# Kernel tuning notes

Measured on AMD Instinct MI355X. Metric: run time of the kernel, lower is better.

## Reference

```python
import math
import jax, jax.numpy as jnp
import numpy as np

B, T, N, FIN, D, H, HM, L, P, O = 8, 12, 512, 3, 128, 4, 256, 3, 12, 1


def _pe(t, d):
    pos = jnp.arange(t, dtype=jnp.float32)[:, None]
    div = jnp.exp(jnp.arange(0, d, 2, dtype=jnp.float32) * (-math.log(10000.0) / d))
    pe = jnp.zeros((t, d), jnp.float32)
    pe = pe.at[:, 0::2].set(jnp.sin(pos * div))
    pe = pe.at[:, 1::2].set(jnp.cos(pos * div))
    return pe


def _spatial_attn(x, qkvW, qkvb, pW, pb):
    # attention over the node axis, per (batch, time)
    b, t, n, d = x.shape
    hd = d // H
    scale = hd ** -0.5
    qkv = jnp.einsum('btnd,ced->cbtne', x, qkvW) + qkvb[:, None, None, None, :]
    q, k, v = [a.reshape(b, t, n, H, hd) for a in qkv]
    a = jax.nn.softmax(jnp.einsum('btihe,btjhe->bthij', q, k) * scale, axis=-1)
    o = jnp.einsum('bthij,btjhe->btihe', a, v).reshape(b, t, n, d)
    return jnp.einsum('btnd,od->btno', o, pW) + pb


def _temporal_attn(x, qkvW, qkvb, pW, pb):
    # attention over the time axis, per (batch, node)
    b, t, n, d = x.shape
    hd = d // H
    scale = hd ** -0.5
    qkv = jnp.einsum('btnd,ced->cbtne', x, qkvW) + qkvb[:, None, None, None, :]
    q, k, v = [a.reshape(b, t, n, H, hd) for a in qkv]
    a = jax.nn.softmax(jnp.einsum('bxnhe,bynhe->bnhxy', q, k) * scale, axis=-1)
    o = jnp.einsum('bnhxy,bynhe->bxnhe', a, v).reshape(b, t, n, d)
    return jnp.einsum('btnd,od->btno', o, pW) + pb


def _layernorm(x, g, b, eps=1e-5):
    mu = x.mean(-1, keepdims=True)
    var = ((x - mu) ** 2).mean(-1, keepdims=True)
    return (x - mu) / jnp.sqrt(var + eps) * g + b


def setup_inputs() -> dict:
    key = jax.random.key(0)
    ks = iter(jax.random.split(key, 40))
    s = 0.02
    rn = lambda shape: jax.random.normal(next(ks), shape, jnp.float32) * s
    inp = {
        'x': jax.random.normal(next(ks), (B, T, N, FIN), jnp.float32),
        'tok_W': rn((D, FIN)), 'tok_b': rn((D,)),
        't_qkvW': rn((L, 3, D, D)), 't_qkvb': rn((L, 3, D)),
        't_pW': rn((L, D, D)), 't_pb': rn((L, D)),
        'g_qkvW': rn((L, 3, D, D)), 'g_qkvb': rn((L, 3, D)),
        'g_pW': rn((L, D, D)), 'g_pb': rn((L, D)),
        's_qkvW': rn((L, 3, D, D)), 's_qkvb': rn((L, 3, D)),
        's_pW': rn((L, D, D)), 's_pb': rn((L, D)),
        'resW': rn((L, D, D)), 'resb': rn((L, D)),
        'normW': jnp.ones((L, D), jnp.float32), 'normb': jnp.zeros((L, D), jnp.float32),
        'fc1W': rn((L, HM, 2 * D)), 'fc1b': rn((L, HM)),
        'fc2W': rn((L, D, HM)), 'fc2b': rn((L, D)),
        'end1W': rn((P, T)), 'end1b': rn((P,)),
        'end2W': rn((O, L * D)), 'end2b': rn((O,)),
    }
    return inp


def reference(x, tok_W, tok_b, t_qkvW, t_qkvb, t_pW, t_pb,
              g_qkvW, g_qkvb, g_pW, g_pb, s_qkvW, s_qkvb, s_pW, s_pb,
              resW, resb, normW, normb, fc1W, fc1b, fc2W, fc2b,
              end1W, end1b, end2W, end2b):
    # DataEmbedding: token linear + sinusoidal positional encoding over T
    h = jnp.einsum('btnf,df->btnd', x, tok_W) + tok_b
    h = h + _pe(h.shape[1], h.shape[3])[None, :, None, :]
    outs = []
    for l in range(t_qkvW.shape[0]):
        residual = h
        h = _temporal_attn(h, t_qkvW[l], t_qkvb[l], t_pW[l], t_pb[l])
        geo = _spatial_attn(h, g_qkvW[l], g_qkvb[l], g_pW[l], g_pb[l])
        sem = _spatial_attn(h, s_qkvW[l], s_qkvb[l], s_pW[l], s_pb[l])
        cat = jnp.concatenate([geo, sem], axis=-1)
        m = jax.nn.gelu(jnp.einsum('btnc,hc->btnh', cat, fc1W[l]) + fc1b[l], approximate=False)
        m = jnp.einsum('btnh,oh->btno', m, fc2W[l]) + fc2b[l]
        pre = jnp.einsum('btnd,od->btno', residual, resW[l]) + resb[l] + m
        h = _layernorm(pre, normW[l], normb[l])
        outs.append(h)
    xc = jnp.concatenate(outs, axis=-1)  # [B,T,N,L*D]
    y = jax.nn.relu(jnp.einsum('btnc,pt->bpnc', xc, end1W) + end1b[None, :, None, None])
    y = jnp.einsum('bpnc,oc->bpno', y, end2W) + end2b
    return y  # [B, pred_len, N, output_size]; structure_kl_loss is identically 0
```

## Files before the change

kernel.cpp:

```cpp
#include <hip/hip_runtime.h>
#include <hip/hip_bf16.h>
#include <math.h>

#define BB 8
#define TT 12
#define NN 512
#define FIN 3
#define DD 128
#define HH 4
#define HD 32
#define HMID 256
#define LL 3
#define PP 12
#define BTOK (TT*NN)

typedef short bf16x8 __attribute__((ext_vector_type(8)));
typedef float f32x4  __attribute__((ext_vector_type(4)));

__device__ __forceinline__ unsigned short f2bf(float f) {
    unsigned u = __float_as_uint(f);
    unsigned r = u + 0x7fffu + ((u >> 16) & 1u);
    return (unsigned short)(r >> 16);
}
__device__ __forceinline__ float bf2f(short s) {
    return __uint_as_float((unsigned)(unsigned short)s << 16);
}
__device__ __forceinline__ unsigned pk2bf(float a, float b) {
    __hip_bfloat162 h = __float22bfloat162_rn(make_float2(a, b));
    return *(unsigned*)&h;
}

__global__ __launch_bounds__(256)
void convert_weights_kernel(const float* __restrict__ t_qkvW, const float* __restrict__ t_pW,
                            const float* __restrict__ g_qkvW, const float* __restrict__ g_pW,
                            const float* __restrict__ s_qkvW, const float* __restrict__ s_pW,
                            const float* __restrict__ resW, const float* __restrict__ fc1W,
                            const float* __restrict__ fc2W, short* __restrict__ dst)
{
    int base = (blockIdx.x * 256 + threadIdx.x) * 4;
    const float* src; int off;
    if      (base < 147456) { src = t_qkvW; off = 0; }
    else if (base < 196608) { src = t_pW;   off = 147456; }
    else if (base < 344064) { src = g_qkvW; off = 196608; }
    else if (base < 393216) { src = g_pW;   off = 344064; }
    else if (base < 540672) { src = s_qkvW; off = 393216; }
    else if (base < 589824) { src = s_pW;   off = 540672; }
    else if (base < 638976) { src = resW;   off = 589824; }
    else if (base < 835584) { src = fc1W;   off = 638976; }
    else                    { src = fc2W;   off = 835584; }
    float4 v = *(const float4*)(src + (base - off));
    *(uint2*)(dst + base) = make_uint2(pk2bf(v.x, v.y), pk2bf(v.z, v.w));
}

__global__ __launch_bounds__(256)
void combine_weights_kernel(const float* __restrict__ g_qkvW, const float* __restrict__ s_qkvW,
                            const float* __restrict__ t_pW, const float* __restrict__ g_pW,
                            const float* __restrict__ s_pW, const float* __restrict__ g_qkvb,
                            const float* __restrict__ s_qkvb, const float* __restrict__ t_pb,
                            const float* __restrict__ g_pb, const float* __restrict__ s_pb,
                            const float* __restrict__ fc1W, const float* __restrict__ fc1b,
                            short* __restrict__ wbf, float* __restrict__ qkvb2,
                            float* __restrict__ fc1b2)
{
    __shared__ float Bs[128][128];
    const int tid = threadIdx.x;
    const int blk = blockIdx.x;
    const float* A; const float* B; int arst;
    short* outp; int orst;
    int l, sel, c = 0, half = 0;
    const bool isqkv = blk < 18;
    if (isqkv) {
        l = blk / 6; int r = blk % 6; sel = r / 3; c = r % 3;
        A = (sel ? s_qkvW : g_qkvW) + (size_t)(l*3 + c) * 16384;  arst = 128;
        B = t_pW + (size_t)l * 16384;
        outp = wbf + (sel ? 393216 : 196608) + (size_t)l*49152 + (size_t)c*16384;
        orst = 128;
    } else {
        int r = blk - 18; l = r / 4; r %= 4; sel = r >> 1; half = r & 1;
        A = fc1W + (size_t)(l*256 + half*128) * 256 + sel*128;    arst = 256;
        B = (sel ? s_pW : g_pW) + (size_t)l * 16384;
        outp = wbf + 638976 + (size_t)l*65536 + (size_t)half*32768 + sel*128;
        orst = 256;
    }
    for (int idx = tid; idx < 16384; idx += 256)
        Bs[idx >> 7][idx & 127] = B[idx];
    __syncthreads();

    const int e = tid >> 1, db = (tid & 1) * 64;
    const float* Arow = A + (size_t)e * arst;
    #pragma unroll 1
    for (int ch = 0; ch < 4; ++ch) {
        float acc[16] = {};
        for (int o4 = 0; o4 < 32; ++o4) {
            float4 a4 = *(const float4*)(Arow + o4*4);
            float as[4] = {a4.x, a4.y, a4.z, a4.w};
            #pragma unroll
            for (int k = 0; k < 4; ++k) {
                #pragma unroll
                for (int j4 = 0; j4 < 4; ++j4) {
                    float4 b = *(const float4*)&Bs[o4*4 + k][db + ch*16 + j4*4];
                    acc[j4*4+0] += as[k]*b.x;
                    acc[j4*4+1] += as[k]*b.y;
                    acc[j4*4+2] += as[k]*b.z;
                    acc[j4*4+3] += as[k]*b.w;
                }
            }
        }
        short* orow = outp + (size_t)e * orst + db + ch*16;
        #pragma unroll
        for (int j = 0; j < 8; ++j)
            ((unsigned*)orow)[j] = pk2bf(acc[2*j], acc[2*j+1]);
    }

    if (tid < 128) {
        if (isqkv) {
            const float* tb = t_pb + l*128;
            const float* ar = A + (size_t)tid * 128;
            float s = (sel ? s_qkvb : g_qkvb)[(l*3 + c)*128 + tid];
            for (int o = 0; o < 128; ++o) s += ar[o] * tb[o];
            qkvb2[l*768 + sel*384 + c*128 + tid] = s;
        } else if (sel == 0) {
            int hg = half*128 + tid;
            const float* frow = fc1W + (size_t)(l*256 + hg) * 256;
            const float* gb = g_pb + l*128;
            const float* sb = s_pb + l*128;
            float s = fc1b[l*256 + hg];
            for (int o = 0; o < 128; ++o) s += frow[o]*gb[o] + frow[128+o]*sb[o];
            fc1b2[l*256 + hg] = s;
        }
    }
}

__global__ __launch_bounds__(256)
void embed_kernel(const float* __restrict__ x, const float* __restrict__ tokW,
                  const float* __restrict__ tokb, short* __restrict__ h)
{
    int gid = blockIdx.x * 256 + threadIdx.x;
    int d = gid & (DD - 1);
    int token = gid >> 7;
    int t = (token / NN) % TT;
    const float* xp = x + (size_t)token * FIN;
    float v = tokb[d] + xp[0]*tokW[d*3+0] + xp[1]*tokW[d*3+1] + xp[2]*tokW[d*3+2];
    int de = d & ~1;
    float freq = __expf(-(float)de * (9.210340371976184f / (float)DD));
    float ang = (float)t * freq;
    v += (d & 1) ? cosf(ang) : sinf(ang);
    h[gid] = (short)f2bf(v);
}

template<int ACT, bool OBF16>
__device__ __forceinline__ void gemm_core(
    const short* __restrict__ Ap, int lda, const short* __restrict__ W, int K,
    const float* __restrict__ bias, const float* __restrict__ addsrc, int ald,
    void* __restrict__ outp, int ldc)
{
    __shared__ __align__(16) short As[64][72];
    __shared__ __align__(16) short Bs[128][72];
    const int tid = threadIdx.x;
    const int lane = tid & 63, w = tid >> 6;
    const int wm = (w & 1) * 32, wn = (w >> 1) * 64;
    const int l15 = lane & 15, lq = lane >> 4;
    f32x4 acc[2][4] = {};
    const int arow = tid >> 2, achk = (tid & 3) * 16;
    const int brow = tid >> 1, bchk = (tid & 1) * 32;

    for (int k0 = 0; k0 < K; k0 += 64) {
        const short* ap = Ap + (size_t)arow * lda + k0 + achk;
        *(uint4*)&As[arow][achk]     = *(const uint4*)ap;
        *(uint4*)&As[arow][achk + 8] = *(const uint4*)(ap + 8);
        const short* wp = W + (size_t)brow * K + k0 + bchk;
        #pragma unroll
        for (int i = 0; i < 4; ++i)
            *(uint4*)&Bs[brow][bchk + i*8] = *(const uint4*)(wp + i*8);
        __syncthreads();
        #pragma unroll
        for (int kc = 0; kc < 2; ++kc) {
            bf16x8 af[2], bfv[4];
            #pragma unroll
            for (int mi = 0; mi < 2; ++mi)
                af[mi] = *(const bf16x8*)&As[wm + mi*16 + l15][kc*32 + lq*8];
            #pragma unroll
            for (int nj = 0; nj < 4; ++nj)
                bfv[nj] = *(const bf16x8*)&Bs[wn + nj*16 + l15][kc*32 + lq*8];
            #pragma unroll
            for (int mi = 0; mi < 2; ++mi)
                #pragma unroll
                for (int nj = 0; nj < 4; ++nj)
                    acc[mi][nj] = __builtin_amdgcn_mfma_f32_16x16x32_bf16(
                        af[mi], bfv[nj], acc[mi][nj], 0, 0, 0);
        }
        __syncthreads();
    }

    #pragma unroll
    for (int nj = 0; nj < 4; ++nj) {
        int col = wn + nj * 16 + l15;
        float bv = bias[col];
        #pragma unroll
        for (int mi = 0; mi < 2; ++mi) {
            #pragma unroll
            for (int r = 0; r < 4; ++r) {
                int row = wm + mi * 16 + lq * 4 + r;
                float v = acc[mi][nj][r] + bv;
                if (addsrc) v += addsrc[(size_t)row * ald + col];
                if (ACT == 1) v = 0.5f * v * (1.0f + erff(v * 0.7071067811865476f));
                if (OBF16) ((short*)outp)[(size_t)row * ldc + col] = (short)f2bf(v);
                else       ((float*)outp)[(size_t)row * ldc + col] = v;
            }
        }
    }
}

template<int ACT, bool OBF16>
__global__ __launch_bounds__(256)
void gemm_plain(const short* __restrict__ A, const short* __restrict__ W,
                const float* __restrict__ bias, const float* __restrict__ addsrc,
                void* __restrict__ out, int K, int lda, int ldc, int ald)
{
    size_t bm = (size_t)blockIdx.x * 64;
    int bn = blockIdx.y * 128;
    void* op = OBF16 ? (void*)((short*)out + bm * ldc + bn)
                     : (void*)((float*)out + bm * ldc + bn);
    const float* ad = addsrc ? addsrc + bm * ald + bn : nullptr;
    gemm_core<ACT, OBF16>(A + bm * lda, lda, W + (size_t)bn * K, K, bias + bn,
                          ad, ald, op, ldc);
}

__global__ __launch_bounds__(256)
void gemm_qkv_gs(const short* __restrict__ A, const short* __restrict__ W1,
                 const short* __restrict__ W2, const float* __restrict__ b1,
                 const float* __restrict__ b2, short* __restrict__ out)
{
    size_t bm = (size_t)blockIdx.x * 64;
    int y = blockIdx.y;
    const short* W = (y < 3) ? W1 : W2;
    const float* b = (y < 3) ? b1 : b2;
    int wc = ((y < 3) ? y : y - 3) * 128;
    gemm_core<0, true>(A + bm * 128, 128, W + (size_t)wc * 128, 128,
                       b + wc, nullptr, 0, out + bm * 768 + y * 128, 768);
}

__global__ __launch_bounds__(192)
void temporal_attn_kernel(const short* __restrict__ qkv, short* __restrict__ out)
{
    __shared__ __align__(16) short kvs[4][TT][264];
    const int tid = threadIdx.x;
    const int bn0 = blockIdx.x * 4;

    #pragma unroll
    for (int i = 0; i < 8; ++i) {
        int flat = (i*192 + tid) * 8;
        int ns = flat / 3072;
        int rem = flat - ns*3072;
        int t = rem >> 8, c = rem & 255;
        int bn = bn0 + ns;
        int b = bn >> 9, n = bn & (NN - 1);
        const short* src = qkv + ((size_t)(b*TT + t) * NN + n) * 384 + 128 + c;
        *(uint4*)&kvs[ns][t][c] = *(const uint4*)src;
    }

    const int nsub = tid / 48;
    const int r = tid - nsub*48;
    const int h = r / TT, ti = r - h*TT;
    const int bn = bn0 + nsub;
    const int b = bn >> 9, n = bn & (NN - 1);
    const float qscale = 0.17677669529663687f * 1.4426950408889634f;

    float q[32];
    {
        const short* qp = qkv + ((size_t)(b*TT + ti) * NN + n) * 384 + h*HD;
        #pragma unroll
        for (int i = 0; i < 16; ++i) {
            unsigned u = ((const unsigned*)qp)[i];
            q[2*i]   = __uint_as_float(u << 16) * qscale;
            q[2*i+1] = __uint_as_float(u & 0xffff0000u) * qscale;
        }
    }
    __syncthreads();

    float s[TT];
    #pragma unroll
    for (int tj = 0; tj < TT; ++tj) {
        const unsigned* kr = (const unsigned*)&kvs[nsub][tj][h*HD];
        float d0 = 0.f, d1 = 0.f;
        #pragma unroll
        for (int i = 0; i < 16; ++i) {
            unsigned u = kr[i];
            d0 += q[2*i]   * __uint_as_float(u << 16);
            d1 += q[2*i+1] * __uint_as_float(u & 0xffff0000u);
        }
        s[tj] = d0 + d1;
    }
    float sum = 0.f, p[TT];
    #pragma unroll
    for (int tj = 0; tj < TT; ++tj) { p[tj] = __builtin_amdgcn_exp2f(s[tj]); sum += p[tj]; }
    float inv = 1.f / sum;

    float o[32];
    #pragma unroll
    for (int e = 0; e < 32; ++e) o[e] = 0.f;
    #pragma unroll
    for (int tj = 0; tj < TT; ++tj) {
        const unsigned* vr = (const unsigned*)&kvs[nsub][tj][128 + h*HD];
        float pj = p[tj];
        #pragma unroll
        for (int i = 0; i < 16; ++i) {
            unsigned u = vr[i];
            o[2*i]   += pj * __uint_as_float(u << 16);
            o[2*i+1] += pj * __uint_as_float(u & 0xffff0000u);
        }
    }

    short* op = out + ((size_t)(b*TT + ti) * NN + n) * DD + h*HD;
    #pragma unroll
    for (int i = 0; i < 16; ++i)
        ((unsigned*)op)[i] = pk2bf(o[2*i] * inv, o[2*i+1] * inv);
}

__global__ __launch_bounds__(256)
void spatial_attn_mfma_kernel(const short* __restrict__ qkv, short* __restrict__ out)
{
    __shared__ __align__(16) short Qs[128][40];
    __shared__ __align__(16) short Ks[64][40];
    __shared__ __align__(16) short Vt[36][72];
    __shared__ __align__(16) short Ps[4][32][72];

    const int tid = threadIdx.x;
    const int bid = blockIdx.x;
    const int sel = bid & 1;
    const int qb = (bid >> 1) & 3;
    const int h = (bid >> 3) & 3;
    const int bt = bid >> 5;
    const int lane = tid & 63, w = tid >> 6;
    const int l15 = lane & 15, lq = lane >> 4;

    const size_t btbase = (size_t)bt * NN * 768 + sel * 384 + h * HD;
    const float qscale = 0.17677669529663687f * 1.4426950408889634f;

    {
        int r = tid >> 1, hf = (tid & 1) * 16;
        const unsigned* qp = (const unsigned*)(qkv + btbase + (size_t)(qb*128 + r) * 768 + hf);
        unsigned tmp[8];
        #pragma unroll
        for (int i = 0; i < 8; ++i) {
            unsigned u = qp[i];
            tmp[i] = pk2bf(__uint_as_float(u << 16) * qscale,
                           __uint_as_float(u & 0xffff0000u) * qscale);
        }
        *(uint4*)&Qs[r][hf]     = *(const uint4*)tmp;
        *(uint4*)&Qs[r][hf + 8] = *(const uint4*)(tmp + 4);
    }
    for (int idx = tid; idx < 4*72; idx += 256) {
        int rr = idx / 72, cc = idx - rr*72;
        Vt[32 + rr][cc] = (rr == 0 && cc < 64) ? (short)0x3F80 : (short)0;
    }

    f32x4 acc_o[2][3] = {};
    const int ve = tid & 31, vkb = (tid >> 5) * 8;

    for (int kt = 0; kt < 8; ++kt) {
        __syncthreads();
        {
            int r = tid >> 2, c = (tid & 3) * 8;
            const short* kp = qkv + btbase + (size_t)(kt*64 + r) * 768 + 128 + c;
            *(uint4*)&Ks[r][c] = *(const uint4*)kp;
        }
        {
            const short* vp = qkv + btbase + (size_t)(kt*64 + vkb) * 768 + 256 + ve;
            short tmp[8];
            #pragma unroll
            for (int jj = 0; jj < 8; ++jj) tmp[jj] = vp[(size_t)jj * 768];
            *(uint4*)&Vt[ve][vkb] = *(const uint4*)tmp;
        }
        __syncthreads();

        bf16x8 kf[4], qf[2];
        #pragma unroll
        for (int km = 0; km < 4; ++km)
            kf[km] = *(const bf16x8*)&Ks[km*16 + l15][lq*8];
        #pragma unroll
        for (int qn = 0; qn < 2; ++qn)
            qf[qn] = *(const bf16x8*)&Qs[w*32 + qn*16 + l15][lq*8];
        f32x4 sacc[4][2] = {};
        #pragma unroll
        for (int km = 0; km < 4; ++km)
            #pragma unroll
            for (int qn = 0; qn < 2; ++qn)
                sacc[km][qn] = __builtin_amdgcn_mfma_f32_16x16x32_bf16(
                    kf[km], qf[qn], sacc[km][qn], 0, 0, 0);

        #pragma unroll
        for (int km = 0; km < 4; ++km)
            #pragma unroll
            for (int qn = 0; qn < 2; ++qn) {
                float e0 = __builtin_amdgcn_exp2f(sacc[km][qn][0]);
                float e1 = __builtin_amdgcn_exp2f(sacc[km][qn][1]);
                float e2 = __builtin_amdgcn_exp2f(sacc[km][qn][2]);
                float e3 = __builtin_amdgcn_exp2f(sacc[km][qn][3]);
                *(uint2*)&Ps[w][qn*16 + l15][km*16 + lq*4] =
                    make_uint2(pk2bf(e0, e1), pk2bf(e2, e3));
            }

        #pragma unroll
        for (int kk = 0; kk < 2; ++kk) {
            bf16x8 pa[2], vb[3];
            #pragma unroll
            for (int mi = 0; mi < 2; ++mi)
                pa[mi] = *(const bf16x8*)&Ps[w][mi*16 + l15][kk*32 + lq*8];
            #pragma unroll
            for (int nj = 0; nj < 3; ++nj)
                vb[nj] = *(const bf16x8*)&Vt[nj*16 + l15][kk*32 + lq*8];
            #pragma unroll
            for (int mi = 0; mi < 2; ++mi)
                #pragma unroll
                for (int nj = 0; nj < 3; ++nj)
                    acc_o[mi][nj] = __builtin_amdgcn_mfma_f32_16x16x32_bf16(
                        pa[mi], vb[nj], acc_o[mi][nj], 0, 0, 0);
        }
    }

    #pragma unroll
    for (int mi = 0; mi < 2; ++mi) {
        #pragma unroll
        for (int r = 0; r < 4; ++r) {
            float l = __shfl(acc_o[mi][2][r], lane & 48);
            float inv = 1.f / l;
            int qrow = qb*128 + w*32 + mi*16 + lq*4 + r;
            short* op = out + ((size_t)bt * NN + qrow) * 256 + sel*128 + h*HD;
            op[l15]      = (short)f2bf(acc_o[mi][0][r] * inv);
            op[16 + l15] = (short)f2bf(acc_o[mi][1][r] * inv);
        }
    }
}

__global__ __launch_bounds__(256)
void layernorm_kernel(const float* __restrict__ in, const float* __restrict__ g,
                      const float* __restrict__ bta, short* __restrict__ outh,
                      float* __restrict__ xc, int lcol)
{
    int tid = threadIdx.x;
    int wave = tid >> 6, lane = tid & 63;
    size_t token = (size_t)blockIdx.x * 4 + wave;
    const float* row = in + token * DD;
    float x0 = row[lane], x1 = row[lane + 64];
    float s = x0 + x1, ss = x0*x0 + x1*x1;
    #pragma unroll
    for (int off = 1; off < 64; off <<= 1) {
        s  += __shfl_xor(s,  off);
        ss += __shfl_xor(ss, off);
    }
    float mu = s * (1.f / DD);
    float var = ss * (1.f / DD) - mu * mu;
    float rstd = rsqrtf(var + 1e-5f);
    float y0 = (x0 - mu) * rstd * g[lane]      + bta[lane];
    float y1 = (x1 - mu) * rstd * g[lane + 64] + bta[lane + 64];
    outh[token*DD + lane]      = (short)f2bf(y0);
    outh[token*DD + lane + 64] = (short)f2bf(y1);
    xc[token*(LL*DD) + lcol + lane]      = y0;
    xc[token*(LL*DD) + lcol + lane + 64] = y1;
}

__global__ __launch_bounds__(256)
void head_kernel(const float* __restrict__ xc, const float* __restrict__ e1W,
                 const float* __restrict__ e1b, const float* __restrict__ e2W,
                 const float* __restrict__ e2b, float* __restrict__ out)
{
    __shared__ float xcs[TT][LL*DD];
    __shared__ float w1[PP*TT];
    int bid = blockIdx.x;
    int b = bid >> 9, n = bid & (NN - 1);
    int tid = threadIdx.x;
    if (tid < PP*TT) w1[tid] = e1W[tid];
    #pragma unroll
    for (int i = 0; i < 18; ++i) {
        int f = i*256 + tid;
        int t = f / (LL*DD), c = f % (LL*DD);
        xcs[t][c] = xc[(((size_t)(b*TT + t) * NN) + n) * (LL*DD) + c];
    }
    __syncthreads();
    int p = tid >> 4, lane16 = tid & 15;
    float acc = 0.f;
    if (p < PP) {
        for (int c = lane16; c < LL*DD; c += 16) {
            float tmp = e1b[p];
            #pragma unroll
            for (int t = 0; t < TT; ++t) tmp += xcs[t][c] * w1[p*TT + t];
            tmp = fmaxf(tmp, 0.f);
            acc += tmp * e2W[c];
        }
    }
    acc += __shfl_xor(acc, 1);
    acc += __shfl_xor(acc, 2);
    acc += __shfl_xor(acc, 4);
    acc += __shfl_xor(acc, 8);
    if (p < PP && lane16 == 0)
        out[((size_t)(b*PP + p)) * NN + n] = acc + e2b[0];
}

extern "C" void kernel_launch(void* const* d_in, const int* in_sizes, int n_in,
                              void* d_out, int out_size, void* d_ws, size_t ws_size,
                              hipStream_t stream)
{
    const float* x      = (const float*)d_in[0];
    const float* tok_W  = (const float*)d_in[1];
    const float* tok_b  = (const float*)d_in[2];
    const float* t_qkvW = (const float*)d_in[3];
    const float* t_qkvb = (const float*)d_in[4];
    const float* t_pW   = (const float*)d_in[5];
    const float* t_pb   = (const float*)d_in[6];
    const float* g_qkvW = (const float*)d_in[7];
    const float* g_qkvb = (const float*)d_in[8];
    const float* g_pW   = (const float*)d_in[9];
    const float* g_pb   = (const float*)d_in[10];
    const float* s_qkvW = (const float*)d_in[11];
    const float* s_qkvb = (const float*)d_in[12];
    const float* s_pW   = (const float*)d_in[13];
    const float* s_pb   = (const float*)d_in[14];
    const float* resW   = (const float*)d_in[15];
    const float* resb   = (const float*)d_in[16];
    const float* normW  = (const float*)d_in[17];
    const float* normb  = (const float*)d_in[18];
    const float* fc1W   = (const float*)d_in[19];
    const float* fc1b   = (const float*)d_in[20];
    const float* fc2W   = (const float*)d_in[21];
    const float* fc2b   = (const float*)d_in[22];
    const float* end1W  = (const float*)d_in[23];
    const float* end1b  = (const float*)d_in[24];
    const float* end2W  = (const float*)d_in[25];
    const float* end2b  = (const float*)d_in[26];
    float* out = (float*)d_out;

    short* wbf = (short*)d_ws;
    const size_t WBF = 933888;
    float* qkvb2 = (float*)(wbf + WBF);
    float* fc1b2 = qkvb2 + 2304;
    short* act   = (short*)(fc1b2 + 768);

    convert_weights_kernel<<<912, 256, 0, stream>>>(
        t_qkvW, t_pW, g_qkvW, g_pW, s_qkvW, s_pW, resW, fc1W, fc2W, wbf);
    combine_weights_kernel<<<30, 256, 0, stream>>>(
        g_qkvW, s_qkvW, t_pW, g_pW, s_pW, g_qkvb, s_qkvb, t_pb, g_pb, s_pb,
        fc1W, fc1b, wbf, qkvb2, fc1b2);

    const size_t fixedBytes = WBF*2 + 3072*4;
    const size_t perBatchBytes = (size_t)BTOK * 2432 * 2;
    int nb = 8;
    while (nb > 1 && fixedBytes + (size_t)nb * perBatchBytes > ws_size) nb >>= 1;

    for (int b0 = 0; b0 < BB; b0 += nb) {
        const int CT = nb * BTOK;
        const int GM = CT / 64;
        short* h    = act;
        short* qkvh = h + (size_t)CT*128;
        short* m1   = qkvh;
        short* atmp = qkvh + (size_t)CT*768;
        float* m2   = (float*)(atmp + (size_t)CT*256);
        float* pre  = m2 + (size_t)CT*128;
        float* xc   = pre + (size_t)CT*128;

        const float* xch = x + (size_t)b0 * BTOK * FIN;
        float* outch = out + (size_t)b0 * PP * NN;

        embed_kernel<<<CT*DD/256, 256, 0, stream>>>(xch, tok_W, tok_b, h);

        for (int l = 0; l < LL; ++l) {
            const short* tqw = wbf + 0      + (size_t)l*49152;
            const short* gqw = wbf + 196608 + (size_t)l*49152;
            const short* sqw = wbf + 393216 + (size_t)l*49152;
            const short* rsw = wbf + 589824 + (size_t)l*16384;
            const short* f1w = wbf + 638976 + (size_t)l*65536;
            const short* f2w = wbf + 835584 + (size_t)l*32768;
            const float* tqb = t_qkvb + (size_t)l*384;

            gemm_plain<0,true><<<dim3(GM,3), 256, 0, stream>>>(
                h, tqw, tqb, nullptr, qkvh, 128, 128, 384, 0);
            temporal_attn_kernel<<<nb*NN/4, 192, 0, stream>>>(qkvh, atmp);

            gemm_qkv_gs<<<dim3(GM,6), 256, 0, stream>>>(
                atmp, gqw, sqw, qkvb2 + l*768, qkvb2 + l*768 + 384, qkvh);
            spatial_attn_mfma_kernel<<<nb*TT*HH*4*2, 256, 0, stream>>>(qkvh, atmp);

            gemm_plain<1,true><<<dim3(GM,2), 256, 0, stream>>>(
                atmp, f1w, fc1b2 + l*256, nullptr, m1, 256, 256, 256, 0);
            gemm_plain<0,false><<<dim3(GM,1), 256, 0, stream>>>(
                m1, f2w, fc2b + (size_t)l*128, nullptr, m2, 256, 256, 128, 0);
            gemm_plain<0,false><<<dim3(GM,1), 256, 0, stream>>>(
                h, rsw, resb + (size_t)l*128, m2, pre, 128, 128, 128, 128);
            layernorm_kernel<<<CT/4, 256, 0, stream>>>(pre, normW + (size_t)l*128,
                                                       normb + (size_t)l*128, h, xc, l*DD);
        }

        head_kernel<<<nb*NN, 256, 0, stream>>>(xc, end1W, end1b, end2W, end2b, outch);
    }
}
```

Before: 769.5 us.

## Fuse fc2, residual projection and layernorm into one K-concatenated GEMM kernel

Lays out the fc1 output and the hidden state side by side in a single [token,384] buffer and builds a combined [fc2W | resW] weight. One GEMM with K=384 then computes fc2 plus the residual projection, and its epilogue applies LayerNorm directly. This removes two GEMM launches, the fp32 m2 and pre intermediates, and the separate layernorm pass. It also pads the spatial-attention shared-memory tiles, likely to reduce bank conflicts. The cost is a cross-wave reduction through shared memory inside the GEMM epilogue, and in-place overwriting of the hidden-state columns of the shared buffer.

```diff
diff --git a/kernel.cpp b/kernel.cpp
--- a/kernel.cpp
+++ b/kernel.cpp
@@ -38,6 +38,16 @@
                             const float* __restrict__ fc2W, short* __restrict__ dst)
 {
     int base = (blockIdx.x * 256 + threadIdx.x) * 4;
+    if (base >= 933888) {
+        int idx = base - 933888;
+        int l = idx / 49152, r2 = idx - l*49152;
+        int d = r2 / 384, col = r2 - d*384;
+        const float* s2 = (col < 256) ? fc2W + ((size_t)(l*128 + d))*256 + col
+                                      : resW + ((size_t)(l*128 + d))*128 + (col - 256);
+        float4 v = *(const float4*)s2;
+        *(uint2*)(dst + base) = make_uint2(pk2bf(v.x, v.y), pk2bf(v.z, v.w));
+        return;
+    }
     const float* src; int off;
     if      (base < 147456) { src = t_qkvW; off = 0; }
     else if (base < 196608) { src = t_pW;   off = 147456; }
@@ -133,7 +143,7 @@
 
 __global__ __launch_bounds__(256)
 void embed_kernel(const float* __restrict__ x, const float* __restrict__ tokW,
-                  const float* __restrict__ tokb, short* __restrict__ h)
+                  const float* __restrict__ tokb, short* __restrict__ cat2)
 {
     int gid = blockIdx.x * 256 + threadIdx.x;
     int d = gid & (DD - 1);
@@ -145,14 +155,13 @@
     float freq = __expf(-(float)de * (9.210340371976184f / (float)DD));
     float ang = (float)t * freq;
     v += (d & 1) ? cosf(ang) : sinf(ang);
-    h[gid] = (short)f2bf(v);
+    cat2[(size_t)token * 384 + 256 + d] = (short)f2bf(v);
 }
 
 template<int ACT, bool OBF16>
 __device__ __forceinline__ void gemm_core(
     const short* __restrict__ Ap, int lda, const short* __restrict__ W, int K,
-    const float* __restrict__ bias, const float* __restrict__ addsrc, int ald,
-    void* __restrict__ outp, int ldc)
+    const float* __restrict__ bias, void* __restrict__ outp, int ldc)
 {
     __shared__ __align__(16) short As[64][72];
     __shared__ __align__(16) short Bs[128][72];
@@ -202,7 +211,6 @@
             for (int r = 0; r < 4; ++r) {
                 int row = wm + mi * 16 + lq * 4 + r;
                 float v = acc[mi][nj][r] + bv;
-                if (addsrc) v += addsrc[(size_t)row * ald + col];
                 if (ACT == 1) v = 0.5f * v * (1.0f + erff(v * 0.7071067811865476f));
                 if (OBF16) ((short*)outp)[(size_t)row * ldc + col] = (short)f2bf(v);
                 else       ((float*)outp)[(size_t)row * ldc + col] = v;
@@ -214,16 +222,14 @@
 template<int ACT, bool OBF16>
 __global__ __launch_bounds__(256)
 void gemm_plain(const short* __restrict__ A, const short* __restrict__ W,
-                const float* __restrict__ bias, const float* __restrict__ addsrc,
-                void* __restrict__ out, int K, int lda, int ldc, int ald)
+                const float* __restrict__ bias, void* __restrict__ out,
+                int K, int lda, int ldc)
 {
     size_t bm = (size_t)blockIdx.x * 64;
     int bn = blockIdx.y * 128;
     void* op = OBF16 ? (void*)((short*)out + bm * ldc + bn)
                      : (void*)((float*)out + bm * ldc + bn);
-    const float* ad = addsrc ? addsrc + bm * ald + bn : nullptr;
-    gemm_core<ACT, OBF16>(A + bm * lda, lda, W + (size_t)bn * K, K, bias + bn,
-                          ad, ald, op, ldc);
+    gemm_core<ACT, OBF16>(A + bm * lda, lda, W + (size_t)bn * K, K, bias + bn, op, ldc);
 }
 
 __global__ __launch_bounds__(256)
@@ -237,7 +243,108 @@
     const float* b = (y < 3) ? b1 : b2;
     int wc = ((y < 3) ? y : y - 3) * 128;
     gemm_core<0, true>(A + bm * 128, 128, W + (size_t)wc * 128, 128,
-                       b + wc, nullptr, 0, out + bm * 768 + y * 128, 768);
+                       b + wc, out + bm * 768 + y * 128, 768);
+}
+
+__global__ __launch_bounds__(256)
+void gemm_ln_kernel(const short* __restrict__ cat2, const short* __restrict__ Wc,
+                    const float* __restrict__ fc2b, const float* __restrict__ resb,
+                    const float* __restrict__ g, const float* __restrict__ bta,
+                    short* __restrict__ cat2out, float* __restrict__ xc, int lcol)
+{
+    __shared__ __align__(16) short As[64][72];
+    __shared__ __align__(16) short Bs[128][72];
+    __shared__ float rsum[64][2], rssq[64][2];
+    const int tid = threadIdx.x;
+    const int lane = tid & 63, w = tid >> 6;
+    const int wm = (w & 1) * 32, wn = (w >> 1) * 64;
+    const int l15 = lane & 15, lq = lane >> 4;
+    const size_t bm = (size_t)blockIdx.x * 64;
+    f32x4 acc[2][4] = {};
+    const int arow = tid >> 2, achk = (tid & 3) * 16;
+    const int brow = tid >> 1, bchk = (tid & 1) * 32;
+    const short* Ap = cat2 + bm * 384;
+
+    for (int k0 = 0; k0 < 384; k0 += 64) {
+        const short* ap = Ap + (size_t)arow * 384 + k0 + achk;
+        *(uint4*)&As[arow][achk]     = *(const uint4*)ap;
+        *(uint4*)&As[arow][achk + 8] = *(const uint4*)(ap + 8);
+        const short* wp = Wc + (size_t)brow * 384 + k0 + bchk;
+        #pragma unroll
+        for (int i = 0; i < 4; ++i)
+            *(uint4*)&Bs[brow][bchk + i*8] = *(const uint4*)(wp + i*8);
+        __syncthreads();
+        #pragma unroll
+        for (int kc = 0; kc < 2; ++kc) {
+            bf16x8 af[2], bfv[4];
+            #pragma unroll
+            for (int mi = 0; mi < 2; ++mi)
+                af[mi] = *(const bf16x8*)&As[wm + mi*16 + l15][kc*32 + lq*8];
+            #pragma unroll
+            for (int nj = 0; nj < 4; ++nj)
+                bfv[nj] = *(const bf16x8*)&Bs[wn + nj*16 + l15][kc*32 + lq*8];
+            #pragma unroll
+            for (int mi = 0; mi < 2; ++mi)
+                #pragma unroll
+                for (int nj = 0; nj < 4; ++nj)
+                    acc[mi][nj] = __builtin_amdgcn_mfma_f32_16x16x32_bf16(
+                        af[mi], bfv[nj], acc[mi][nj], 0, 0, 0);
+        }
+        __syncthreads();
+    }
+
+    float vv[2][4][4];
+    float ps[2][4] = {}, pq[2][4] = {};
+    #pragma unroll
+    for (int nj = 0; nj < 4; ++nj) {
+        int col = wn + nj * 16 + l15;
+        float bv = fc2b[col] + resb[col];
+        #pragma unroll
+        for (int mi = 0; mi < 2; ++mi)
+            #pragma unroll
+            for (int r = 0; r < 4; ++r) {
+                float v = acc[mi][nj][r] + bv;
+                vv[mi][nj][r] = v;
+                ps[mi][r] += v;
+                pq[mi][r] += v * v;
+            }
+    }
+    #pragma unroll
+    for (int mi = 0; mi < 2; ++mi)
+        #pragma unroll
+        for (int r = 0; r < 4; ++r) {
+            #pragma unroll
+            for (int off = 1; off < 16; off <<= 1) {
+                ps[mi][r] += __shfl_xor(ps[mi][r], off);
+                pq[mi][r] += __shfl_xor(pq[mi][r], off);
+            }
+            if (l15 == 0) {
+                int row = wm + mi*16 + lq*4 + r;
+                rsum[row][w >> 1] = ps[mi][r];
+                rssq[row][w >> 1] = pq[mi][r];
+            }
+        }
+    __syncthreads();
+
+    #pragma unroll
+    for (int mi = 0; mi < 2; ++mi)
+        #pragma unroll
+        for (int r = 0; r < 4; ++r) {
+            int row = wm + mi*16 + lq*4 + r;
+            float s = rsum[row][0] + rsum[row][1];
+            float ss = rssq[row][0] + rssq[row][1];
+            float mu = s * (1.f / DD);
+            float var = ss * (1.f / DD) - mu * mu;
+            float rstd = rsqrtf(var + 1e-5f);
+            size_t grow = bm + row;
+            #pragma unroll
+            for (int nj = 0; nj < 4; ++nj) {
+                int col = wn + nj * 16 + l15;
+                float y = (vv[mi][nj][r] - mu) * rstd * g[col] + bta[col];
+                cat2out[grow * 384 + 256 + col] = (short)f2bf(y);
+                xc[grow * 384 + lcol + col] = y;
+            }
+        }
 }
 
 __global__ __launch_bounds__(192)
@@ -322,8 +429,8 @@
 {
     __shared__ __align__(16) short Qs[128][40];
     __shared__ __align__(16) short Ks[64][40];
-    __shared__ __align__(16) short Vt[36][72];
-    __shared__ __align__(16) short Ps[4][32][72];
+    __shared__ __align__(16) short Vt[36][88];
+    __shared__ __align__(16) short Ps[4][32][88];
 
     const int tid = threadIdx.x;
     const int bid = blockIdx.x;
@@ -350,8 +457,8 @@
         *(uint4*)&Qs[r][hf]     = *(const uint4*)tmp;
         *(uint4*)&Qs[r][hf + 8] = *(const uint4*)(tmp + 4);
     }
-    for (int idx = tid; idx < 4*72; idx += 256) {
-        int rr = idx / 72, cc = idx - rr*72;
+    for (int idx = tid; idx < 4*88; idx += 256) {
+        int rr = idx / 88, cc = idx - rr*88;
         Vt[32 + rr][cc] = (rr == 0 && cc < 64) ? (short)0x3F80 : (short)0;
     }
 
@@ -431,33 +538,6 @@
             op[16 + l15] = (short)f2bf(acc_o[mi][1][r] * inv);
         }
     }
-}
-
-__global__ __launch_bounds__(256)
-void layernorm_kernel(const float* __restrict__ in, const float* __restrict__ g,
-                      const float* __restrict__ bta, short* __restrict__ outh,
-                      float* __restrict__ xc, int lcol)
-{
-    int tid = threadIdx.x;
-    int wave = tid >> 6, lane = tid & 63;
-    size_t token = (size_t)blockIdx.x * 4 + wave;
-    const float* row = in + token * DD;
-    float x0 = row[lane], x1 = row[lane + 64];
-    float s = x0 + x1, ss = x0*x0 + x1*x1;
-    #pragma unroll
-    for (int off = 1; off < 64; off <<= 1) {
-        s  += __shfl_xor(s,  off);
-        ss += __shfl_xor(ss, off);
-    }
-    float mu = s * (1.f / DD);
-    float var = ss * (1.f / DD) - mu * mu;
-    float rstd = rsqrtf(var + 1e-5f);
-    float y0 = (x0 - mu) * rstd * g[lane]      + bta[lane];
-    float y1 = (x1 - mu) * rstd * g[lane + 64] + bta[lane + 64];
-    outh[token*DD + lane]      = (short)f2bf(y0);
-    outh[token*DD + lane + 64] = (short)f2bf(y1);
-    xc[token*(LL*DD) + lcol + lane]      = y0;
-    xc[token*(LL*DD) + lcol + lane + 64] = y1;
 }
 
 __global__ __launch_bounds__(256)
@@ -531,49 +611,45 @@
     float* out = (float*)d_out;
 
     short* wbf = (short*)d_ws;
-    const size_t WBF = 933888;
+    const size_t WBF = 1081344;
     float* qkvb2 = (float*)(wbf + WBF);
     float* fc1b2 = qkvb2 + 2304;
     short* act   = (short*)(fc1b2 + 768);
 
-    convert_weights_kernel<<<912, 256, 0, stream>>>(
+    convert_weights_kernel<<<1056, 256, 0, stream>>>(
         t_qkvW, t_pW, g_qkvW, g_pW, s_qkvW, s_pW, resW, fc1W, fc2W, wbf);
     combine_weights_kernel<<<30, 256, 0, stream>>>(
         g_qkvW, s_qkvW, t_pW, g_pW, s_pW, g_qkvb, s_qkvb, t_pb, g_pb, s_pb,
         fc1W, fc1b, wbf, qkvb2, fc1b2);
 
     const size_t fixedBytes = WBF*2 + 3072*4;
-    const size_t perBatchBytes = (size_t)BTOK * 2432 * 2;
+    const size_t perBatchBytes = (size_t)BTOK * 4352;
     int nb = 8;
     while (nb > 1 && fixedBytes + (size_t)nb * perBatchBytes > ws_size) nb >>= 1;
 
     for (int b0 = 0; b0 < BB; b0 += nb) {
         const int CT = nb * BTOK;
         const int GM = CT / 64;
-        short* h    = act;
-        short* qkvh = h + (size_t)CT*128;
-        short* m1   = qkvh;
+        short* cat2 = act;
+        short* qkvh = cat2 + (size_t)CT*384;
         short* atmp = qkvh + (size_t)CT*768;
-        float* m2   = (float*)(atmp + (size_t)CT*256);
-        float* pre  = m2 + (size_t)CT*128;
-        float* xc   = pre + (size_t)CT*128;
+        float* xc   = (float*)(atmp + (size_t)CT*256);
 
         const float* xch = x + (size_t)b0 * BTOK * FIN;
         float* outch = out + (size_t)b0 * PP * NN;
 
-        embed_kernel<<<CT*DD/256, 256, 0, stream>>>(xch, tok_W, tok_b, h);
+        embed_kernel<<<CT*DD/256, 256, 0, stream>>>(xch, tok_W, tok_b, cat2);
 
         for (int l = 0; l < LL; ++l) {
             const short* tqw = wbf + 0      + (size_t)l*49152;
             const short* gqw = wbf + 196608 + (size_t)l*49152;
             const short* sqw = wbf + 393216 + (size_t)l*49152;
-            const short* rsw = wbf + 589824 + (size_t)l*16384;
             const short* f1w = wbf + 638976 + (size_t)l*65536;
-            const short* f2w = wbf + 835584 + (size_t)l*32768;
+            const short* f2rw= wbf + 933888 + (size_t)l*49152;
             const float* tqb = t_qkvb + (size_t)l*384;
 
             gemm_plain<0,true><<<dim3(GM,3), 256, 0, stream>>>(
-                h, tqw, tqb, nullptr, qkvh, 128, 128, 384, 0);
+                cat2 + 256, tqw, tqb, qkvh, 128, 384, 384);
             temporal_attn_kernel<<<nb*NN/4, 192, 0, stream>>>(qkvh, atmp);
 
             gemm_qkv_gs<<<dim3(GM,6), 256, 0, stream>>>(
@@ -581,13 +657,10 @@
             spatial_attn_mfma_kernel<<<nb*TT*HH*4*2, 256, 0, stream>>>(qkvh, atmp);
 
             gemm_plain<1,true><<<dim3(GM,2), 256, 0, stream>>>(
-                atmp, f1w, fc1b2 + l*256, nullptr, m1, 256, 256, 256, 0);
-            gemm_plain<0,false><<<dim3(GM,1), 256, 0, stream>>>(
-                m1, f2w, fc2b + (size_t)l*128, nullptr, m2, 256, 256, 128, 0);
-            gemm_plain<0,false><<<dim3(GM,1), 256, 0, stream>>>(
-                h, rsw, resb + (size_t)l*128, m2, pre, 128, 128, 128, 128);
-            layernorm_kernel<<<CT/4, 256, 0, stream>>>(pre, normW + (size_t)l*128,
-                                                       normb + (size_t)l*128, h, xc, l*DD);
+                atmp, f1w, fc1b2 + l*256, cat2, 256, 256, 384);
+            gemm_ln_kernel<<<GM, 256, 0, stream>>>(
+                cat2, f2rw, fc2b + (size_t)l*128, resb + (size_t)l*128,
+                normW + (size_t)l*128, normb + (size_t)l*128, cat2, xc, l*DD);
         }
 
         head_kernel<<<nb*NN, 256, 0, stream>>>(xc, end1W, end1b, end2W, end2b, outch);
```

After: 716.1 us. 6.9% less time.
